# Performance work log

Measured on AMD Instinct MI355X. Metric: run time of the kernel, lower is better.

Reference implementation:

```python
import jax, jax.numpy as jnp
import numpy as np

N_NODES = 100000
IN_DIM = 128
N_HEADS = 4
D_HEAD = 32
N_EDGES = 800000
LN_EPS = 1e-5
NEG_SLOPE = 0.2


def setup_inputs() -> dict:
    key = jax.random.key(0)
    k = jax.random.split(key, 7)
    x = jax.random.normal(k[0], (N_NODES, IN_DIM), dtype=jnp.float32)
    edge_index = jax.random.randint(k[1], (2, N_EDGES), 0, N_NODES, dtype=jnp.int32)
    # W: Linear(in_dim, H*D, bias=False) -> store as [in_dim, H*D] for x @ W
    W = jax.random.normal(k[2], (IN_DIM, N_HEADS * D_HEAD), dtype=jnp.float32) * (1.0 / np.sqrt(IN_DIM))
    # attn_mlp: Linear(2*D, 1, bias=False), shared across heads; split into src/dst halves
    a_src = jax.random.normal(k[3], (D_HEAD,), dtype=jnp.float32) * 0.1
    a_dst = jax.random.normal(k[4], (D_HEAD,), dtype=jnp.float32) * 0.1
    ln_gamma = jnp.ones((N_HEADS * D_HEAD,), dtype=jnp.float32)
    ln_beta = jnp.zeros((N_HEADS * D_HEAD,), dtype=jnp.float32)
    return {"x": x, "edge_index": edge_index, "W": W, "a_src": a_src,
            "a_dst": a_dst, "ln_gamma": ln_gamma, "ln_beta": ln_beta}


def reference(x, edge_index, W, a_src, a_dst, ln_gamma, ln_beta):
    N = x.shape[0]
    # dense projection: [N, H*D] -> [N, H, D]
    h = (x @ W).reshape(N, N_HEADS, D_HEAD)
    src, dst = edge_index[0], edge_index[1]
    h_src = h[src]          # [E, H, D] gather
    h_dst = h[dst]          # [E, H, D] gather
    # attn_mlp(cat([h_src, h_dst])) == h_src @ a[:D] + h_dst @ a[D:]
    s = jnp.einsum('ehd,d->eh', h_src, a_src) + jnp.einsum('ehd,d->eh', h_dst, a_dst)
    s = jnp.where(s > 0, s, NEG_SLOPE * s)  # LeakyReLU(0.2)
    # segment softmax over destination node groups (per head)
    smax = jax.ops.segment_max(s, dst, num_segments=N)          # [N, H]
    e = jnp.exp(s - smax[dst])                                   # [E, H]
    denom = jax.ops.segment_sum(e, dst, num_segments=N)          # [N, H]
    alpha = e / denom[dst]                                       # [E, H]
    # weighted scatter-add aggregation
    msg = h_src * alpha[..., None]                               # [E, H, D]
    out = jax.ops.segment_sum(msg, dst, num_segments=N)          # [N, H, D]
    out = out.reshape(N, N_HEADS * D_HEAD)
    # residual: in_dim == H*D -> Identity
    out = out + x
    # LayerNorm
    mu = out.mean(-1, keepdims=True)
    var = ((out - mu) ** 2).mean(-1, keepdims=True)
    out = (out - mu) / jnp.sqrt(var + LN_EPS) * ln_gamma + ln_beta
    # ELU
    return jnp.where(out > 0, out, jnp.expm1(out))
```

## Files before the change

### kernel.cpp

```cpp
#include <hip/hip_runtime.h>
#include <math.h>

#define NEG_SLOPE 0.2f
#define LN_EPS 1e-5f

#define NB 196
#define EPB 2048
#define SRC_BITS 17
#define NSH 8
#define SCAP 768
#define CURLINE 16
#define SMEM_BYTES (36 * 1024)

typedef __attribute__((ext_vector_type(8))) short bf16x8;
typedef __attribute__((ext_vector_type(4))) float f32x4;

static __device__ __forceinline__ unsigned short f2bf(float f) {
  unsigned u = __float_as_uint(f);
  u += 0x7fffu + ((u >> 16) & 1u);
  return (unsigned short)(u >> 16);
}
static __device__ __forceinline__ unsigned pack_bf16(float a, float b) {
  unsigned ua = __float_as_uint(a);
  unsigned ub = __float_as_uint(b);
  ua += 0x7fffu + ((ua >> 16) & 1u);
  ub += 0x7fffu + ((ub >> 16) & 1u);
  return (ua >> 16) | (ub & 0xffff0000u);
}
static __device__ __forceinline__ float bf_lo(unsigned u) { return __uint_as_float(u << 16); }
static __device__ __forceinline__ float bf_hi(unsigned u) { return __uint_as_float(u & 0xffff0000u); }

__global__ __launch_bounds__(256) void k_scatprep(
    const float* __restrict__ W, const float* __restrict__ a_src,
    const float* __restrict__ a_dst, short* __restrict__ wfrag,
    short* __restrict__ wafrag,
    const int* __restrict__ e_src, const int* __restrict__ e_dst,
    int* __restrict__ cursors, unsigned* __restrict__ ebuf, int n_edges)
{
  __shared__ int hist[NB];
  __shared__ int base[NB];
  const int t = threadIdx.x;
  if (blockIdx.x < 8) {
    const int idx  = blockIdx.x * 256 + t;
    const int tile = idx >> 6;
    const int l2   = idx & 63;
    const int c    = tile >> 2;
    const int kk   = tile & 3;
    const int q2   = l2 >> 4;
    const int i2   = l2 & 15;
    const float* wp = W + (size_t)(kk * 32 + q2 * 8) * 128 + c * 16 + i2;
    bf16x8 wv;
    #pragma unroll
    for (int j = 0; j < 8; ++j) wv[j] = (short)f2bf(wp[(size_t)j * 128]);
    *(bf16x8*)(wfrag + (size_t)idx * 8) = wv;
  } else if (blockIdx.x == 8) {
    const int kk = t >> 6;
    const int l2 = t & 63;
    const int q2 = l2 >> 4;
    const int i2 = l2 & 15;
    bf16x8 wv = {0, 0, 0, 0, 0, 0, 0, 0};
    if (i2 < 8) {
      const int head = i2 >> 1;
      const float* ap = (i2 & 1) ? a_dst : a_src;
      #pragma unroll
      for (int j = 0; j < 8; ++j) {
        const int k = kk * 32 + q2 * 8 + j;
        const float* wr = W + (size_t)k * 128 + head * 32;
        float sum = 0.f;
        for (int d = 0; d < 32; d += 4) {
          const float4 wq = *(const float4*)(wr + d);
          const float4 aq = *(const float4*)(ap + d);
          sum += wq.x * aq.x + wq.y * aq.y + wq.z * aq.z + wq.w * aq.w;
        }
        wv[j] = (short)f2bf(sum);
      }
    }
    *(bf16x8*)(wafrag + (size_t)t * 8) = wv;
  } else {
    const int b = blockIdx.x - 9;
    const int shard = b & (NSH - 1);
    if (t < NB) hist[t] = 0;
    __syncthreads();
    const int e0 = b * EPB + t * 8;
    int n = n_edges - e0;
    n = n < 0 ? 0 : (n > 8 ? 8 : n);
    int da[8], sa[8];
    if (n == 8) {
      const int4 D0 = *(const int4*)(e_dst + e0);
      const int4 D1 = *(const int4*)(e_dst + e0 + 4);
      const int4 S0 = *(const int4*)(e_src + e0);
      const int4 S1 = *(const int4*)(e_src + e0 + 4);
      da[0] = D0.x; da[1] = D0.y; da[2] = D0.z; da[3] = D0.w;
      da[4] = D1.x; da[5] = D1.y; da[6] = D1.z; da[7] = D1.w;
      sa[0] = S0.x; sa[1] = S0.y; sa[2] = S0.z; sa[3] = S0.w;
      sa[4] = S1.x; sa[5] = S1.y; sa[6] = S1.z; sa[7] = S1.w;
    } else {
      #pragma unroll
      for (int i = 0; i < 8; ++i) {
        da[i] = (i < n) ? e_dst[e0 + i] : 0;
        sa[i] = (i < n) ? e_src[e0 + i] : 0;
      }
    }
    int bu[8], rk[8];
    #pragma unroll
    for (int i = 0; i < 8; ++i) {
      bu[i] = da[i] >> 9;
      rk[i] = (i < n) ? atomicAdd(&hist[bu[i]], 1) : 0;
    }
    __syncthreads();
    if (t < NB && hist[t] > 0)
      base[t] = atomicAdd(&cursors[(t * NSH + shard) * CURLINE], hist[t]);
    __syncthreads();
    #pragma unroll
    for (int i = 0; i < 8; ++i) {
      if (i < n) {
        const int pos = base[bu[i]] + rk[i];
        if (pos < SCAP)
          ebuf[((size_t)bu[i] * NSH + shard) * SCAP + pos] =
              ((unsigned)(da[i] & 511) << SRC_BITS) | (unsigned)sa[i];
      }
    }
  }
}

static __device__ __forceinline__ void proj_body(
    const float* __restrict__ x, const short* __restrict__ wfrag,
    const short* __restrict__ wafrag, unsigned* __restrict__ h,
    float* __restrict__ sc, int n_nodes, int pb, char* smem)
{
  short* wlds  = (short*)smem;
  short* walds = (short*)(smem + 32 * 1024);

  const int t    = threadIdx.x;
  const int l    = t & 63;
  const int il   = l & 15;
  const int quad = l >> 4;
  const int wbase = pb * 128 + (t >> 6) * 32;

  {
    const uint4* wf4 = (const uint4*)wfrag;
    uint4* wl4 = (uint4*)wlds;
    #pragma unroll
    for (int i = 0; i < 8; ++i) wl4[t + i * 256] = wf4[t + i * 256];
    ((uint4*)walds)[t] = ((const uint4*)wafrag)[t];
  }
  __syncthreads();

  f32x4 acc[2][8] = {};
  f32x4 acc2[2] = {};
  #pragma unroll
  for (int kk = 0; kk < 4; ++kk) {
    bf16x8 ahi[2], alo[2];
    #pragma unroll
    for (int rt = 0; rt < 2; ++rt) {
      int row = wbase + rt * 16 + il;
      if (row > n_nodes - 1) row = n_nodes - 1;
      const float* p = x + (size_t)row * 128 + kk * 32 + quad * 8;
      const float4 u0 = *(const float4*)(p);
      const float4 u1 = *(const float4*)(p + 4);
      const float f[8] = {u0.x, u0.y, u0.z, u0.w, u1.x, u1.y, u1.z, u1.w};
      #pragma unroll
      for (int j = 0; j < 8; ++j) {
        const unsigned u = __float_as_uint(f[j]);
        ahi[rt][j] = (short)(u >> 16);
        const float lof = f[j] - __uint_as_float(u & 0xffff0000u);
        alo[rt][j] = (short)f2bf(lof);
      }
    }
    #pragma unroll
    for (int c = 0; c < 8; ++c) {
      const bf16x8 bv = *(const bf16x8*)(wlds + ((c * 4 + kk) * 64 + l) * 8);
      acc[0][c] = __builtin_amdgcn_mfma_f32_16x16x32_bf16(ahi[0], bv, acc[0][c], 0, 0, 0);
      acc[0][c] = __builtin_amdgcn_mfma_f32_16x16x32_bf16(alo[0], bv, acc[0][c], 0, 0, 0);
      acc[1][c] = __builtin_amdgcn_mfma_f32_16x16x32_bf16(ahi[1], bv, acc[1][c], 0, 0, 0);
      acc[1][c] = __builtin_amdgcn_mfma_f32_16x16x32_bf16(alo[1], bv, acc[1][c], 0, 0, 0);
    }
    const bf16x8 bv = *(const bf16x8*)(walds + (kk * 64 + l) * 8);
    acc2[0] = __builtin_amdgcn_mfma_f32_16x16x32_bf16(ahi[0], bv, acc2[0], 0, 0, 0);
    acc2[0] = __builtin_amdgcn_mfma_f32_16x16x32_bf16(alo[0], bv, acc2[0], 0, 0, 0);
    acc2[1] = __builtin_amdgcn_mfma_f32_16x16x32_bf16(ahi[1], bv, acc2[1], 0, 0, 0);
    acc2[1] = __builtin_amdgcn_mfma_f32_16x16x32_bf16(alo[1], bv, acc2[1], 0, 0, 0);
  }

  #pragma unroll
  for (int rt = 0; rt < 2; ++rt) {
    #pragma unroll
    for (int reg = 0; reg < 4; ++reg) {
      const int r = wbase + rt * 16 + quad * 4 + reg;
      const bool inb = (r < n_nodes);
      const bool wr = inb && ((il & 3) == 0);
      #pragma unroll
      for (int c = 0; c < 8; ++c) {
        const float v  = acc[rt][c][reg];
        const float vn = __shfl_xor(v, 1);
        const float plo = (il & 1) ? vn : v;
        const float phi = (il & 1) ? v : vn;
        const unsigned px = pack_bf16(plo, phi);
        const unsigned py = __shfl_xor(px, 2);
        if (wr) {
          uint2 u; u.x = px; u.y = py;
          *(uint2*)(h + (size_t)r * 64 + c * 8 + (il >> 1)) = u;
        }
      }
      if (inb && il < 8) sc[(size_t)r * 8 + il] = acc2[rt][reg];
    }
  }
}

static __device__ __forceinline__ void bcsr_body(
    const unsigned* __restrict__ ebuf, const int* __restrict__ cursors,
    int* __restrict__ row_start, int* __restrict__ csr_src, int n_nodes,
    int b, char* smem)
{
  int* sdata = (int*)smem;
  int* hist  = (int*)(smem + 1024);
  int* cur   = (int*)(smem + 3072);
  int* scnt  = (int*)(smem + 5120);
  const int t = threadIdx.x;
  const int n0 = b << 9;

  if (t < NSH) {
    int c = cursors[(b * NSH + t) * CURLINE];
    scnt[t] = c < SCAP ? c : SCAP;
  }
  int tv = 0;
  if (t < NB) {
    #pragma unroll
    for (int s = 0; s < NSH; ++s) {
      int c = cursors[(t * NSH + s) * CURLINE];
      tv += (c < SCAP ? c : SCAP);
    }
  }
  sdata[t] = tv;
  __syncthreads();
  for (int off = 1; off < 256; off <<= 1) {
    const int addv = (t >= off) ? sdata[t - off] : 0;
    __syncthreads();
    sdata[t] += addv;
    __syncthreads();
  }
  const int base = (b == 0) ? 0 : sdata[b - 1];

  hist[t] = 0; hist[t + 256] = 0;
  __syncthreads();
  for (int s = 0; s < NSH; ++s) {
    const unsigned* sl = ebuf + ((size_t)b * NSH + s) * SCAP;
    const int ns = scnt[s];
    for (int e = t; e < ns; e += 256)
      atomicAdd(&hist[sl[e] >> SRC_BITS], 1);
  }
  __syncthreads();

  const int h0 = hist[2 * t], h1 = hist[2 * t + 1];
  const int tsum = h0 + h1;
  sdata[t] = tsum;
  __syncthreads();
  for (int off = 1; off < 256; off <<= 1) {
    const int addv = (t >= off) ? sdata[t - off] : 0;
    __syncthreads();
    sdata[t] += addv;
    __syncthreads();
  }
  const int excl = sdata[t] - tsum;
  cur[2 * t]     = excl;
  cur[2 * t + 1] = excl + h0;
  if (n0 + 2 * t     <= n_nodes) row_start[n0 + 2 * t]     = base + excl;
  if (n0 + 2 * t + 1 <= n_nodes) row_start[n0 + 2 * t + 1] = base + excl + h0;
  __syncthreads();

  for (int s = 0; s < NSH; ++s) {
    const unsigned* sl = ebuf + ((size_t)b * NSH + s) * SCAP;
    const int ns = scnt[s];
    for (int e = t; e < ns; e += 256) {
      const unsigned ds = sl[e];
      const int r = atomicAdd(&cur[ds >> SRC_BITS], 1);
      csr_src[base + r] = (int)(ds & ((1u << SRC_BITS) - 1u));
    }
  }
}

__global__ __launch_bounds__(256, 4) void k_bcsrproj(
    const unsigned* __restrict__ ebuf, const int* __restrict__ cursors,
    int* __restrict__ row_start, int* __restrict__ csr_src, int n_nodes,
    const float* __restrict__ x, const short* __restrict__ wfrag,
    const short* __restrict__ wafrag, unsigned* __restrict__ h,
    float* __restrict__ sc)
{
  __shared__ __align__(16) char smem[SMEM_BYTES];
  if ((int)blockIdx.x < NB)
    bcsr_body(ebuf, cursors, row_start, csr_src, n_nodes, blockIdx.x, smem);
  else
    proj_body(x, wfrag, wafrag, h, sc, n_nodes, (int)blockIdx.x - NB, smem);
}

__global__ __launch_bounds__(256) void k_bcsr(
    const unsigned* __restrict__ ebuf, const int* __restrict__ cursors,
    int* __restrict__ row_start, int* __restrict__ csr_src, int n_nodes)
{
  __shared__ __align__(16) char smem[8 * 1024];
  bcsr_body(ebuf, cursors, row_start, csr_src, n_nodes, blockIdx.x, smem);
}

__global__ __launch_bounds__(256, 4) void k_proj(
    const float* __restrict__ x, const short* __restrict__ wfrag,
    const short* __restrict__ wafrag, unsigned* __restrict__ h,
    float* __restrict__ sc, int n_nodes)
{
  __shared__ __align__(16) char smem[SMEM_BYTES];
  proj_body(x, wfrag, wafrag, h, sc, n_nodes, blockIdx.x, smem);
}

#define ACC_EDGE(al, hv)                              \
  acc[0] = fmaf(al, bf_lo(hv.x), acc[0]);             \
  acc[1] = fmaf(al, bf_hi(hv.x), acc[1]);             \
  acc[2] = fmaf(al, bf_lo(hv.y), acc[2]);             \
  acc[3] = fmaf(al, bf_hi(hv.y), acc[3]);             \
  acc[4] = fmaf(al, bf_lo(hv.z), acc[4]);             \
  acc[5] = fmaf(al, bf_hi(hv.z), acc[5]);             \
  acc[6] = fmaf(al, bf_lo(hv.w), acc[6]);             \
  acc[7] = fmaf(al, bf_hi(hv.w), acc[7]);

__global__ __launch_bounds__(256) void k_agg(
    const unsigned* __restrict__ h, const float* __restrict__ sc,
    const int* __restrict__ row_start, const int* __restrict__ csr_src,
    const float* __restrict__ x, const float* __restrict__ gamma,
    const float* __restrict__ beta, float* __restrict__ out, int n_nodes)
{
  const int t    = threadIdx.x;
  const int lane = t & 63;
  const int g    = lane & 15;
  const int node = blockIdx.x * 16 + (t >> 6) * 4 + (lane >> 4);
  if (node >= n_nodes) return;
  const int head = g >> 2;
  const int sub  = g & 3;
  const int hh   = head * 2;
  const int beg  = row_start[node];
  const int deg  = row_start[node + 1] - beg;

  float acc[8] = {0.f, 0.f, 0.f, 0.f, 0.f, 0.f, 0.f, 0.f};

  if (deg > 0) {
    const float sdv = sc[node * 8 + hh + 1];
    const int dm1 = deg - 1;
    const int j0 = beg + (sub      <= dm1 ? sub      : dm1);
    const int j1 = beg + (sub + 4  <= dm1 ? sub + 4  : dm1);
    const int j2 = beg + (sub + 8  <= dm1 ? sub + 8  : dm1);
    const int j3 = beg + (sub + 12 <= dm1 ? sub + 12 : dm1);
    const int c0 = csr_src[j0];
    const int c1 = csr_src[j1];
    const int c2 = csr_src[j2];
    const int c3 = csr_src[j3];
    float s0 = sc[c0 * 8 + hh];
    float s1 = sc[c1 * 8 + hh];
    float s2 = sc[c2 * 8 + hh];
    float s3 = sc[c3 * 8 + hh];
    s0 += sdv;  s0 = s0 > 0.f ? s0 : NEG_SLOPE * s0;
    s1 += sdv;  s1 = s1 > 0.f ? s1 : NEG_SLOPE * s1;
    s2 += sdv;  s2 = s2 > 0.f ? s2 : NEG_SLOPE * s2;
    s3 += sdv;  s3 = s3 > 0.f ? s3 : NEG_SLOPE * s3;
    const float t0 = (sub      < deg) ? s0 : -INFINITY;
    const float t1 = (sub + 4  < deg) ? s1 : -INFINITY;
    const float t2 = (sub + 8  < deg) ? s2 : -INFINITY;
    const float t3 = (sub + 12 < deg) ? s3 : -INFINITY;
    float m = fmaxf(fmaxf(t0, t1), fmaxf(t2, t3));
    for (int i = sub + 16; i < deg; i += 4) {
      const int cs = csr_src[beg + i];
      float s = sc[cs * 8 + hh] + sdv;  s = s > 0.f ? s : NEG_SLOPE * s;
      m = fmaxf(m, s);
    }
    m = fmaxf(m, __shfl_xor(m, 1));
    m = fmaxf(m, __shfl_xor(m, 2));

    const float e0 = __expf(t0 - m), e1 = __expf(t1 - m);
    const float e2 = __expf(t2 - m), e3 = __expf(t3 - m);
    float l = e0 + e1 + e2 + e3;
    for (int i = sub + 16; i < deg; i += 4) {
      const int cs = csr_src[beg + i];
      float s = sc[cs * 8 + hh] + sdv;  s = s > 0.f ? s : NEG_SLOPE * s;
      l += __expf(s - m);
    }
    l += __shfl_xor(l, 1);
    l += __shfl_xor(l, 2);
    const float inv_l = 1.f / l;
    const float a0 = e0 * inv_l;
    const float a1 = e1 * inv_l;
    const float a2 = e2 * inv_l;
    const float a3 = e3 * inv_l;

    const int base3 = lane & 60;

    const int deg16 = deg < 16 ? deg : 16;
    #pragma unroll
    for (int r = 0; r < 4; ++r) {
      if (r * 4 >= deg16) break;
      const float ar = r == 0 ? a0 : r == 1 ? a1 : r == 2 ? a2 : a3;
      const int   cr = r == 0 ? c0 : r == 1 ? c1 : r == 2 ? c2 : c3;
      const float al0 = __shfl(ar, base3 | 0);
      const float al1 = __shfl(ar, base3 | 1);
      const float al2 = __shfl(ar, base3 | 2);
      const float al3 = __shfl(ar, base3 | 3);
      const int   r0  = __shfl(cr, base3 | 0);
      const int   r1  = __shfl(cr, base3 | 1);
      const int   r2  = __shfl(cr, base3 | 2);
      const int   r3  = __shfl(cr, base3 | 3);
      const uint4 hv0 = *(const uint4*)(h + (size_t)r0 * 64 + g * 4);
      const uint4 hv1 = *(const uint4*)(h + (size_t)r1 * 64 + g * 4);
      const uint4 hv2 = *(const uint4*)(h + (size_t)r2 * 64 + g * 4);
      const uint4 hv3 = *(const uint4*)(h + (size_t)r3 * 64 + g * 4);
      ACC_EDGE(al0, hv0)
      ACC_EDGE(al1, hv1)
      ACC_EDGE(al2, hv2)
      ACC_EDGE(al3, hv3)
    }
    for (int i = 16; i < deg; ++i) {
      const int sr = csr_src[beg + i];
      float s = sc[sr * 8 + hh] + sdv;  s = s > 0.f ? s : NEG_SLOPE * s;
      const float al = __expf(s - m) * inv_l;
      const uint4 hv = *(const uint4*)(h + (size_t)sr * 64 + g * 4);
      ACC_EDGE(al, hv)
    }
  }

  const float4 xa = *(const float4*)(x + (size_t)node * 128 + g * 8);
  const float4 xb = *(const float4*)(x + (size_t)node * 128 + g * 8 + 4);
  float rr[8];
  rr[0] = acc[0] + xa.x;  rr[1] = acc[1] + xa.y;
  rr[2] = acc[2] + xa.z;  rr[3] = acc[3] + xa.w;
  rr[4] = acc[4] + xb.x;  rr[5] = acc[5] + xb.y;
  rr[6] = acc[6] + xb.z;  rr[7] = acc[7] + xb.w;
  float s1 = 0.f, s2 = 0.f;
  #pragma unroll
  for (int j = 0; j < 8; ++j) { s1 += rr[j]; s2 += rr[j] * rr[j]; }
  #pragma unroll
  for (int off = 1; off < 16; off <<= 1) {
    s1 += __shfl_xor(s1, off);
    s2 += __shfl_xor(s2, off);
  }
  const float mu   = s1 * (1.f / 128.f);
  const float var  = s2 * (1.f / 128.f) - mu * mu;
  const float rstd = rsqrtf(var + LN_EPS);
  const float4 ga = *(const float4*)(gamma + g * 8);
  const float4 gb = *(const float4*)(gamma + g * 8 + 4);
  const float4 ba = *(const float4*)(beta  + g * 8);
  const float4 bb = *(const float4*)(beta  + g * 8 + 4);
  float4 o0, o1;
  o0.x = (rr[0] - mu) * rstd * ga.x + ba.x;
  o0.y = (rr[1] - mu) * rstd * ga.y + ba.y;
  o0.z = (rr[2] - mu) * rstd * ga.z + ba.z;
  o0.w = (rr[3] - mu) * rstd * ga.w + ba.w;
  o1.x = (rr[4] - mu) * rstd * gb.x + bb.x;
  o1.y = (rr[5] - mu) * rstd * gb.y + bb.y;
  o1.z = (rr[6] - mu) * rstd * gb.z + bb.z;
  o1.w = (rr[7] - mu) * rstd * gb.w + bb.w;
  o0.x = o0.x > 0.f ? o0.x : expm1f(o0.x);
  o0.y = o0.y > 0.f ? o0.y : expm1f(o0.y);
  o0.z = o0.z > 0.f ? o0.z : expm1f(o0.z);
  o0.w = o0.w > 0.f ? o0.w : expm1f(o0.w);
  o1.x = o1.x > 0.f ? o1.x : expm1f(o1.x);
  o1.y = o1.y > 0.f ? o1.y : expm1f(o1.y);
  o1.z = o1.z > 0.f ? o1.z : expm1f(o1.z);
  o1.w = o1.w > 0.f ? o1.w : expm1f(o1.w);
  *(float4*)(out + (size_t)node * 128 + g * 8)     = o0;
  *(float4*)(out + (size_t)node * 128 + g * 8 + 4) = o1;
}

extern "C" void kernel_launch(void* const* d_in, const int* in_sizes, int n_in,
                              void* d_out, int out_size, void* d_ws, size_t ws_size,
                              hipStream_t stream)
{
  const float* x    = (const float*)d_in[0];
  const int*   ei   = (const int*)d_in[1];
  const float* W    = (const float*)d_in[2];
  const float* a_s  = (const float*)d_in[3];
  const float* a_d  = (const float*)d_in[4];
  const float* gam  = (const float*)d_in[5];
  const float* bet  = (const float*)d_in[6];
  float* out = (float*)d_out;

  const int n_nodes = in_sizes[0] / 128;
  const int n_edges = in_sizes[1] / 2;
  const int* e_src = ei;
  const int* e_dst = ei + n_edges;

  const int nblkE = (n_edges + EPB - 1) / EPB;
  const int nproj = (n_nodes + 127) / 128;

  char* p = (char*)d_ws;
  unsigned* h = (unsigned*)p; p += (size_t)n_nodes * 64 * sizeof(unsigned);
  float* sc   = (float*)p;  p += (size_t)n_nodes * 8 * sizeof(float);
  int* row_start = (int*)p; p += (size_t)(n_nodes + 4) * sizeof(int);
  int* csr_src   = (int*)p; p += (size_t)n_edges * sizeof(int);
  short* wfrag   = (short*)p; p += (size_t)2048 * 8 * sizeof(short);
  short* wafrag  = (short*)p; p += (size_t)256 * 8 * sizeof(short);
  p = (char*)(((size_t)p + 255) & ~(size_t)255);
  int* cursors = (int*)p; p += (size_t)NB * NSH * CURLINE * sizeof(int);

  const bool out_scratch =
      ((size_t)out_size >= (size_t)NB * NSH * SCAP * sizeof(unsigned));
  unsigned* ebuf = out_scratch ? (unsigned*)out : (unsigned*)h;

  hipMemsetAsync(cursors, 0, (size_t)NB * NSH * CURLINE * sizeof(int), stream);

  k_scatprep<<<9 + nblkE, 256, 0, stream>>>(W, a_s, a_d, wfrag, wafrag,
                                            e_src, e_dst, cursors, ebuf,
                                            n_edges);
  if (out_scratch) {
    k_bcsrproj<<<NB + nproj, 256, 0, stream>>>(ebuf, cursors, row_start,
                                               csr_src, n_nodes, x, wfrag,
                                               wafrag, h, sc);
  } else {
    k_bcsr<<<NB, 256, 0, stream>>>(ebuf, cursors, row_start, csr_src, n_nodes);
    k_proj<<<nproj, 256, 0, stream>>>(x, wfrag, wafrag, h, sc, n_nodes);
  }
  k_agg<<<(n_nodes + 15) / 16, 256, 0, stream>>>(h, sc, row_start, csr_src,
                                                 x, gam, bet, out, n_nodes);
}
```

Baseline: 186.8 us.

## Fuse edge scatter with projection; build weight fragments per block in LDS

Restructures the pipeline so the edge-bucketing scatter runs in the same launch as the dense projection, with the CSR build moved to a separate kernel afterward. The weight and attention-vector fragments are no longer precomputed into a workspace buffer. Each projection block converts W and a_src/a_dst into bf16 fragments directly in shared memory. This removes the dependency of the projection on a prior prep kernel, but every one of the ~782 projection blocks now redoes the strided W conversion and the attention dot products.

```diff
diff --git a/kernel.cpp b/kernel.cpp
--- a/kernel.cpp
+++ b/kernel.cpp
@@ -30,18 +30,16 @@
 static __device__ __forceinline__ float bf_lo(unsigned u) { return __uint_as_float(u << 16); }
 static __device__ __forceinline__ float bf_hi(unsigned u) { return __uint_as_float(u & 0xffff0000u); }
 
-__global__ __launch_bounds__(256) void k_scatprep(
+static __device__ __forceinline__ void proj_stage_inline(
     const float* __restrict__ W, const float* __restrict__ a_src,
-    const float* __restrict__ a_dst, short* __restrict__ wfrag,
-    short* __restrict__ wafrag,
-    const int* __restrict__ e_src, const int* __restrict__ e_dst,
-    int* __restrict__ cursors, unsigned* __restrict__ ebuf, int n_edges)
-{
-  __shared__ int hist[NB];
-  __shared__ int base[NB];
+    const float* __restrict__ a_dst, char* smem)
+{
+  short* wlds  = (short*)smem;
+  short* walds = (short*)(smem + 32 * 1024);
   const int t = threadIdx.x;
-  if (blockIdx.x < 8) {
-    const int idx  = blockIdx.x * 256 + t;
+  #pragma unroll
+  for (int i = 0; i < 8; ++i) {
+    const int idx  = t + i * 256;
     const int tile = idx >> 6;
     const int l2   = idx & 63;
     const int c    = tile >> 2;
@@ -52,8 +50,9 @@
     bf16x8 wv;
     #pragma unroll
     for (int j = 0; j < 8; ++j) wv[j] = (short)f2bf(wp[(size_t)j * 128]);
-    *(bf16x8*)(wfrag + (size_t)idx * 8) = wv;
-  } else if (blockIdx.x == 8) {
+    *(bf16x8*)(wlds + (size_t)idx * 8) = wv;
+  }
+  {
     const int kk = t >> 6;
     const int l2 = t & 63;
     const int q2 = l2 >> 4;
@@ -75,57 +74,13 @@
         wv[j] = (short)f2bf(sum);
       }
     }
-    *(bf16x8*)(wafrag + (size_t)t * 8) = wv;
-  } else {
-    const int b = blockIdx.x - 9;
-    const int shard = b & (NSH - 1);
-    if (t < NB) hist[t] = 0;
-    __syncthreads();
-    const int e0 = b * EPB + t * 8;
-    int n = n_edges - e0;
-    n = n < 0 ? 0 : (n > 8 ? 8 : n);
-    int da[8], sa[8];
-    if (n == 8) {
-      const int4 D0 = *(const int4*)(e_dst + e0);
-      const int4 D1 = *(const int4*)(e_dst + e0 + 4);
-      const int4 S0 = *(const int4*)(e_src + e0);
-      const int4 S1 = *(const int4*)(e_src + e0 + 4);
-      da[0] = D0.x; da[1] = D0.y; da[2] = D0.z; da[3] = D0.w;
-      da[4] = D1.x; da[5] = D1.y; da[6] = D1.z; da[7] = D1.w;
-      sa[0] = S0.x; sa[1] = S0.y; sa[2] = S0.z; sa[3] = S0.w;
-      sa[4] = S1.x; sa[5] = S1.y; sa[6] = S1.z; sa[7] = S1.w;
-    } else {
-      #pragma unroll
-      for (int i = 0; i < 8; ++i) {
-        da[i] = (i < n) ? e_dst[e0 + i] : 0;
-        sa[i] = (i < n) ? e_src[e0 + i] : 0;
-      }
-    }
-    int bu[8], rk[8];
-    #pragma unroll
-    for (int i = 0; i < 8; ++i) {
-      bu[i] = da[i] >> 9;
-      rk[i] = (i < n) ? atomicAdd(&hist[bu[i]], 1) : 0;
-    }
-    __syncthreads();
-    if (t < NB && hist[t] > 0)
-      base[t] = atomicAdd(&cursors[(t * NSH + shard) * CURLINE], hist[t]);
-    __syncthreads();
-    #pragma unroll
-    for (int i = 0; i < 8; ++i) {
-      if (i < n) {
-        const int pos = base[bu[i]] + rk[i];
-        if (pos < SCAP)
-          ebuf[((size_t)bu[i] * NSH + shard) * SCAP + pos] =
-              ((unsigned)(da[i] & 511) << SRC_BITS) | (unsigned)sa[i];
-      }
-    }
-  }
+    *(bf16x8*)(walds + (size_t)t * 8) = wv;
+  }
+  __syncthreads();
 }
 
 static __device__ __forceinline__ void proj_body(
-    const float* __restrict__ x, const short* __restrict__ wfrag,
-    const short* __restrict__ wafrag, unsigned* __restrict__ h,
+    const float* __restrict__ x, unsigned* __restrict__ h,
     float* __restrict__ sc, int n_nodes, int pb, char* smem)
 {
   short* wlds  = (short*)smem;
@@ -136,15 +91,6 @@
   const int il   = l & 15;
   const int quad = l >> 4;
   const int wbase = pb * 128 + (t >> 6) * 32;
-
-  {
-    const uint4* wf4 = (const uint4*)wfrag;
-    uint4* wl4 = (uint4*)wlds;
-    #pragma unroll
-    for (int i = 0; i < 8; ++i) wl4[t + i * 256] = wf4[t + i * 256];
-    ((uint4*)walds)[t] = ((const uint4*)wafrag)[t];
-  }
-  __syncthreads();
 
   f32x4 acc[2][8] = {};
   f32x4 acc2[2] = {};
@@ -207,16 +153,85 @@
   }
 }
 
-static __device__ __forceinline__ void bcsr_body(
+static __device__ __forceinline__ void scatter_body(
+    const int* __restrict__ e_src, const int* __restrict__ e_dst,
+    int* __restrict__ cursors, unsigned* __restrict__ ebuf, int n_edges,
+    int b, char* smem)
+{
+  int* hist = (int*)smem;
+  int* base = (int*)(smem + 1024);
+  const int t = threadIdx.x;
+  const int shard = b & (NSH - 1);
+  if (t < NB) hist[t] = 0;
+  __syncthreads();
+  const int e0 = b * EPB + t * 8;
+  int n = n_edges - e0;
+  n = n < 0 ? 0 : (n > 8 ? 8 : n);
+  int da[8], sa[8];
+  if (n == 8) {
+    const int4 D0 = *(const int4*)(e_dst + e0);
+    const int4 D1 = *(const int4*)(e_dst + e0 + 4);
+    const int4 S0 = *(const int4*)(e_src + e0);
+    const int4 S1 = *(const int4*)(e_src + e0 + 4);
+    da[0] = D0.x; da[1] = D0.y; da[2] = D0.z; da[3] = D0.w;
+    da[4] = D1.x; da[5] = D1.y; da[6] = D1.z; da[7] = D1.w;
+    sa[0] = S0.x; sa[1] = S0.y; sa[2] = S0.z; sa[3] = S0.w;
+    sa[4] = S1.x; sa[5] = S1.y; sa[6] = S1.z; sa[7] = S1.w;
+  } else {
+    #pragma unroll
+    for (int i = 0; i < 8; ++i) {
+      da[i] = (i < n) ? e_dst[e0 + i] : 0;
+      sa[i] = (i < n) ? e_src[e0 + i] : 0;
+    }
+  }
+  int bu[8], rk[8];
+  #pragma unroll
+  for (int i = 0; i < 8; ++i) {
+    bu[i] = da[i] >> 9;
+    rk[i] = (i < n) ? atomicAdd(&hist[bu[i]], 1) : 0;
+  }
+  __syncthreads();
+  if (t < NB && hist[t] > 0)
+    base[t] = atomicAdd(&cursors[(t * NSH + shard) * CURLINE], hist[t]);
+  __syncthreads();
+  #pragma unroll
+  for (int i = 0; i < 8; ++i) {
+    if (i < n) {
+      const int pos = base[bu[i]] + rk[i];
+      if (pos < SCAP)
+        ebuf[((size_t)bu[i] * NSH + shard) * SCAP + pos] =
+            ((unsigned)(da[i] & 511) << SRC_BITS) | (unsigned)sa[i];
+    }
+  }
+}
+
+__global__ __launch_bounds__(256, 4) void k_scatproj(
+    const int* __restrict__ e_src, const int* __restrict__ e_dst,
+    int* __restrict__ cursors, unsigned* __restrict__ ebuf, int n_edges,
+    int nblk,
+    const float* __restrict__ x, const float* __restrict__ W,
+    const float* __restrict__ a_src, const float* __restrict__ a_dst,
+    unsigned* __restrict__ h, float* __restrict__ sc, int n_nodes)
+{
+  __shared__ __align__(16) char smem[SMEM_BYTES];
+  if ((int)blockIdx.x < nblk) {
+    scatter_body(e_src, e_dst, cursors, ebuf, n_edges, blockIdx.x, smem);
+  } else {
+    proj_stage_inline(W, a_src, a_dst, smem);
+    proj_body(x, h, sc, n_nodes, (int)blockIdx.x - nblk, smem);
+  }
+}
+
+__global__ __launch_bounds__(256) void k_bcsr(
     const unsigned* __restrict__ ebuf, const int* __restrict__ cursors,
-    int* __restrict__ row_start, int* __restrict__ csr_src, int n_nodes,
-    int b, char* smem)
-{
+    int* __restrict__ row_start, int* __restrict__ csr_src, int n_nodes)
+{
+  __shared__ __align__(16) char smem[6 * 1024];
   int* sdata = (int*)smem;
   int* hist  = (int*)(smem + 1024);
   int* cur   = (int*)(smem + 3072);
   int* scnt  = (int*)(smem + 5120);
-  const int t = threadIdx.x;
+  const int b = blockIdx.x, t = threadIdx.x;
   const int n0 = b << 9;
 
   if (t < NSH) {
@@ -279,35 +294,22 @@
   }
 }
 
-__global__ __launch_bounds__(256, 4) void k_bcsrproj(
-    const unsigned* __restrict__ ebuf, const int* __restrict__ cursors,
-    int* __restrict__ row_start, int* __restrict__ csr_src, int n_nodes,
-    const float* __restrict__ x, const short* __restrict__ wfrag,
-    const short* __restrict__ wafrag, unsigned* __restrict__ h,
-    float* __restrict__ sc)
+__global__ __launch_bounds__(256) void k_scat(
+    const int* __restrict__ e_src, const int* __restrict__ e_dst,
+    int* __restrict__ cursors, unsigned* __restrict__ ebuf, int n_edges)
+{
+  __shared__ __align__(16) char smem[2 * 1024];
+  scatter_body(e_src, e_dst, cursors, ebuf, n_edges, blockIdx.x, smem);
+}
+
+__global__ __launch_bounds__(256, 4) void k_proj(
+    const float* __restrict__ x, const float* __restrict__ W,
+    const float* __restrict__ a_src, const float* __restrict__ a_dst,
+    unsigned* __restrict__ h, float* __restrict__ sc, int n_nodes)
 {
   __shared__ __align__(16) char smem[SMEM_BYTES];
-  if ((int)blockIdx.x < NB)
-    bcsr_body(ebuf, cursors, row_start, csr_src, n_nodes, blockIdx.x, smem);
-  else
-    proj_body(x, wfrag, wafrag, h, sc, n_nodes, (int)blockIdx.x - NB, smem);
-}
-
-__global__ __launch_bounds__(256) void k_bcsr(
-    const unsigned* __restrict__ ebuf, const int* __restrict__ cursors,
-    int* __restrict__ row_start, int* __restrict__ csr_src, int n_nodes)
-{
-  __shared__ __align__(16) char smem[8 * 1024];
-  bcsr_body(ebuf, cursors, row_start, csr_src, n_nodes, blockIdx.x, smem);
-}
-
-__global__ __launch_bounds__(256, 4) void k_proj(
-    const float* __restrict__ x, const short* __restrict__ wfrag,
-    const short* __restrict__ wafrag, unsigned* __restrict__ h,
-    float* __restrict__ sc, int n_nodes)
-{
-  __shared__ __align__(16) char smem[SMEM_BYTES];
-  proj_body(x, wfrag, wafrag, h, sc, n_nodes, blockIdx.x, smem);
+  proj_stage_inline(W, a_src, a_dst, smem);
+  proj_body(x, h, sc, n_nodes, blockIdx.x, smem);
 }
 
 #define ACC_EDGE(al, hv)                              \
@@ -490,8 +492,6 @@
   float* sc   = (float*)p;  p += (size_t)n_nodes * 8 * sizeof(float);
   int* row_start = (int*)p; p += (size_t)(n_nodes + 4) * sizeof(int);
   int* csr_src   = (int*)p; p += (size_t)n_edges * sizeof(int);
-  short* wfrag   = (short*)p; p += (size_t)2048 * 8 * sizeof(short);
-  short* wafrag  = (short*)p; p += (size_t)256 * 8 * sizeof(short);
   p = (char*)(((size_t)p + 255) & ~(size_t)255);
   int* cursors = (int*)p; p += (size_t)NB * NSH * CURLINE * sizeof(int);
 
@@ -501,16 +501,15 @@
 
   hipMemsetAsync(cursors, 0, (size_t)NB * NSH * CURLINE * sizeof(int), stream);
 
-  k_scatprep<<<9 + nblkE, 256, 0, stream>>>(W, a_s, a_d, wfrag, wafrag,
-                                            e_src, e_dst, cursors, ebuf,
-                                            n_edges);
   if (out_scratch) {
-    k_bcsrproj<<<NB + nproj, 256, 0, stream>>>(ebuf, cursors, row_start,
-                                               csr_src, n_nodes, x, wfrag,
-                                               wafrag, h, sc);
+    k_scatproj<<<nblkE + nproj, 256, 0, stream>>>(
+        e_src, e_dst, cursors, ebuf, n_edges, nblkE,
+        x, W, a_s, a_d, h, sc, n_nodes);
+    k_bcsr<<<NB, 256, 0, stream>>>(ebuf, cursors, row_start, csr_src, n_nodes);
   } else {
+    k_scat<<<nblkE, 256, 0, stream>>>(e_src, e_dst, cursors, ebuf, n_edges);
     k_bcsr<<<NB, 256, 0, stream>>>(ebuf, cursors, row_start, csr_src, n_nodes);
-    k_proj<<<nproj, 256, 0, stream>>>(x, wfrag, wafrag, h, sc, n_nodes);
+    k_proj<<<nproj, 256, 0, stream>>>(x, W, a_s, a_d, h, sc, n_nodes);
   }
   k_agg<<<(n_nodes + 15) / 16, 256, 0, stream>>>(h, sc, row_start, csr_src,
                                                  x, gam, bet, out, n_nodes);
```

Result: slower. 224.3 us (+20.1%).
